# Kernel tuning notes

Hardware: AMD Instinct MI355X
Metric: run time of the kernel (lower is better)

The kernel has to match this reference:

```python
import jax, jax.numpy as jnp
import numpy as np

W, H = 512, 512
SHIFT_NORM = 100.0
P = 1
WEIGHT = 10.0
EPS = 1e-16


def _cv_matrix(angle, scale, shift, cx, cy):
    # cv2.getRotationMatrix2D-style matrix (pixel coords) with extra x-shift.
    alpha = scale * jnp.cos(angle)
    beta = scale * jnp.sin(angle)
    row0 = jnp.stack([alpha, beta, (1.0 - alpha) * cx - beta * cy + shift], axis=-1)
    row1 = jnp.stack([-beta, alpha, beta * cx + (1.0 - alpha) * cy], axis=-1)
    return jnp.stack([row0, row1], axis=-2)  # [B,2,3]


def _normalize_transform(M, width, height):
    # Convert pixel-space affine to normalized [-1,1] coords (align_corners=True).
    a, b, tx = M[:, 0, 0], M[:, 0, 1], M[:, 0, 2]
    c, d, ty = M[:, 1, 0], M[:, 1, 1], M[:, 1, 2]
    sw = float(width - 1)
    sh = float(height - 1)
    A = a
    Bc = b * sh / sw
    Cc = a + b * sh / sw + 2.0 * tx / sw - 1.0
    D = c * sw / sh
    E = d
    Fc = c * sw / sh + d + 2.0 * ty / sh - 1.0
    row0 = jnp.stack([A, Bc, Cc], axis=-1)
    row1 = jnp.stack([D, E, Fc], axis=-1)
    return jnp.stack([row0, row1], axis=-2)  # [B,2,3]


def _affine_grid(T, height, width):
    # torch affine_grid, align_corners=True
    u = jnp.linspace(-1.0, 1.0, width, dtype=T.dtype)
    v = jnp.linspace(-1.0, 1.0, height, dtype=T.dtype)
    vv, uu = jnp.meshgrid(v, u, indexing='ij')
    base = jnp.stack([uu, vv, jnp.ones_like(uu)], axis=-1)  # [H,W,3]
    return jnp.einsum('bij,hwj->bhwi', T, base)  # [B,H,W,2] (x,y)


def _grid_sample(img, grid):
    # bilinear, zeros padding, align_corners=True. img [B,C,H,W], grid [B,Ho,Wo,2]
    B, C, Hi, Wi = img.shape
    x = (grid[..., 0] + 1.0) * (Wi - 1) / 2.0
    y = (grid[..., 1] + 1.0) * (Hi - 1) / 2.0
    x0 = jnp.floor(x)
    y0 = jnp.floor(y)
    wx1 = x - x0
    wy1 = y - y0
    wx0 = 1.0 - wx1
    wy0 = 1.0 - wy1

    def gather(xi, yi):
        valid = ((xi >= 0) & (xi < Wi) & (yi >= 0) & (yi < Hi)).astype(img.dtype)
        xc = jnp.clip(xi, 0, Wi - 1).astype(jnp.int32)
        yc = jnp.clip(yi, 0, Hi - 1).astype(jnp.int32)
        g = jax.vmap(lambda im, xb, yb, vb: im[:, yb, xb] * vb[None])
        return g(img, xc, yc, valid)  # [B,C,Ho,Wo]

    out = (gather(x0, y0) * (wx0 * wy0)[:, None]
           + gather(x0 + 1, y0) * (wx1 * wy0)[:, None]
           + gather(x0, y0 + 1) * (wx0 * wy1)[:, None]
           + gather(x0 + 1, y0 + 1) * (wx1 * wy1)[:, None])
    return out


def setup_inputs() -> dict:
    key = jax.random.key(0)
    k1, k2, k3 = jax.random.split(key, 3)
    theta = jax.random.normal(k1, (32, 3), dtype=jnp.float32)
    img_R = jax.random.normal(k2, (32, 3, H, W), dtype=jnp.float32)
    img_R_orig = jax.random.normal(k3, (32, 3, H, W), dtype=jnp.float32)
    return {"theta": theta, "img_R": img_R, "img_R_orig": img_R_orig}


def reference(theta, img_R, img_R_orig):
    cx, cy = W // 2, H // 2
    M = _cv_matrix(theta[:, 0], theta[:, 1], SHIFT_NORM * theta[:, 2], cx, cy)
    T = _normalize_transform(M, W, H)
    grid = _affine_grid(T, H, W)
    warped = _grid_sample(img_R_orig, grid)
    mask = jnp.ones((img_R.shape[0], 1, H, W), dtype=img_R.dtype)
    warped_mask = _grid_sample(mask, grid)[:, 0]  # [B,H,W]
    # p=1 norm over channel dim
    nrm = jnp.sum(jnp.abs(img_R - warped), axis=1)  # [B,H,W]
    num = jnp.sum(warped_mask * nrm, axis=(1, 2)) + EPS
    den = jnp.sum(warped_mask, axis=(1, 2)) + EPS
    losses = WEIGHT * num / den
    return jnp.mean(losses)
```

## Files before the change

kernel.cpp:

```cpp
#include <hip/hip_runtime.h>
#include <math.h>

#define IMG_W 512
#define IMG_H 512
#define NB 32
#define NC 3
#define PLANE (IMG_H * IMG_W)

#define TILE_W 32
#define TILE_H 32
#define TILES_X (IMG_W / TILE_W)
#define TILES_Y (IMG_H / TILE_H)
#define TILES_PER_B (TILES_X * TILES_Y)
#define NBLOCKS (NB * TILES_PER_B)

#define LDSC 4096
#define LDSF (3 * LDSC)

typedef float vfloat4 __attribute__((ext_vector_type(4)));


__global__ __launch_bounds__(256, 3) void recon_main(
    const float* __restrict__ theta,
    const float* __restrict__ img_R,
    const float* __restrict__ img_orig,
    float* __restrict__ ws)
{
    __shared__ __align__(16) float tileLds[LDSF + 8];
    __shared__ float snum[4];
    __shared__ float sden[4];

    const int lin  = blockIdx.x;
    const int k    = lin & 7;
    const int i    = lin >> 3;
    const int step = i >> 5;
    const int t    = i & 31;
    const int b    = (4 * k + step) & 31;
    const int chk  = ((b >> 2) - k) & 7;
    const int tile = chk * 32 + t;
    const int tx = (tile & (TILES_X - 1)) * TILE_W;
    const int ty = (tile >> 4) * TILE_H;
    const int gcan = b * TILES_PER_B + tile;

    const int tid  = threadIdx.x;
    const int trow = tid >> 3;
    const int tcol = (tid & 7) * 4;

    const int h  = ty + trow;
    const int w0 = tx + tcol;
    const int p0 = h * IMG_W + w0;

    const float* orig_b = img_orig + (size_t)b * NC * PLANE;
    const float* R_b    = img_R    + (size_t)b * NC * PLANE;

    const vfloat4 rv0 = *(const vfloat4*)(R_b + 0 * PLANE + p0);
    const vfloat4 rv1 = *(const vfloat4*)(R_b + 1 * PLANE + p0);
    const vfloat4 rv2 = *(const vfloat4*)(R_b + 2 * PLANE + p0);

    const float ang   = theta[b * 3 + 0];
    const float s     = theta[b * 3 + 1];
    const float shift = 100.0f * theta[b * 3 + 2];
    float sn, cs;
    sincosf(ang, &sn, &cs);
    const float alpha = s * cs;
    const float beta  = s * sn;
    const float tx_a = (1.0f - alpha) * 256.0f - beta * 256.0f + shift;
    const float ty_a = beta * 256.0f + (1.0f - alpha) * 256.0f;
    const float Cc = alpha + beta + 2.0f * tx_a / 511.0f - 1.0f;
    const float Fc = -beta + alpha + 2.0f * ty_a / 511.0f - 1.0f;
    const float X0 = 255.5f * (Cc + 1.0f - alpha - beta);
    const float Y0 = 255.5f * (Fc + 1.0f + beta - alpha);

    const float xb = X0 + alpha * (float)w0 + beta * (float)h;
    const float yb = Y0 - beta * (float)w0 + alpha * (float)h;

    int   xi0a[4], xi1a[4], yi0a[4], yi1a[4];
    float w00[4], w10[4], w01[4], w11[4], mk[4];
    float den_acc = 0.0f;

#pragma unroll
    for (int j = 0; j < 4; ++j) {
        const float x = xb + alpha * (float)j;
        const float y = yb - beta  * (float)j;
        const float x0f = floorf(x), y0f = floorf(y);
        const float fx1 = x - x0f,  fy1 = y - y0f;
        const float fx0 = 1.0f - fx1, fy0 = 1.0f - fy1;
        const float vx0 = (x0f >=  0.0f && x0f <= 511.0f) ? 1.0f : 0.0f;
        const float vx1 = (x0f >= -1.0f && x0f <= 510.0f) ? 1.0f : 0.0f;
        const float vy0 = (y0f >=  0.0f && y0f <= 511.0f) ? 1.0f : 0.0f;
        const float vy1 = (y0f >= -1.0f && y0f <= 510.0f) ? 1.0f : 0.0f;
        xi0a[j] = (int)fminf(fmaxf(x0f,        0.0f), 511.0f);
        xi1a[j] = (int)fminf(fmaxf(x0f + 1.0f, 0.0f), 511.0f);
        yi0a[j] = (int)fminf(fmaxf(y0f,        0.0f), 511.0f);
        yi1a[j] = (int)fminf(fmaxf(y0f + 1.0f, 0.0f), 511.0f);
        w00[j] = fx0 * fy0 * vx0 * vy0;
        w10[j] = fx1 * fy0 * vx1 * vy0;
        w01[j] = fx0 * fy1 * vx0 * vy1;
        w11[j] = fx1 * fy1 * vx1 * vy1;
        mk[j]  = w00[j] + w10[j] + w01[j] + w11[j];
        den_acc += mk[j];
    }

    const float fx_lo = (float)tx, fx_hi = (float)(tx + TILE_W - 1);
    const float fy_lo = (float)ty, fy_hi = (float)(ty + TILE_H - 1);
    const float cxA = X0 + alpha * fx_lo + beta * fy_lo;
    const float cxB = X0 + alpha * fx_hi + beta * fy_lo;
    const float cxC = X0 + alpha * fx_lo + beta * fy_hi;
    const float cxD = X0 + alpha * fx_hi + beta * fy_hi;
    const float cyA = Y0 - beta * fx_lo + alpha * fy_lo;
    const float cyB = Y0 - beta * fx_hi + alpha * fy_lo;
    const float cyC = Y0 - beta * fx_lo + alpha * fy_hi;
    const float cyD = Y0 - beta * fx_hi + alpha * fy_hi;
    const float min_x = fminf(fminf(cxA, cxB), fminf(cxC, cxD));
    const float max_x = fmaxf(fmaxf(cxA, cxB), fmaxf(cxC, cxD));
    const float min_y = fminf(fminf(cyA, cyB), fminf(cyC, cyD));
    const float max_y = fmaxf(fmaxf(cyA, cyB), fmaxf(cyC, cyD));

    int xlo = (int)floorf(min_x);
    int xhi = (int)floorf(max_x) + 1;
    xlo = min(max(xlo, 0), 511);
    xhi = min(max(xhi, 0), 511);
    xlo &= ~3;
    int ylo = (int)floorf(min_y);
    int yhi = (int)floorf(max_y) + 1;
    ylo = min(max(ylo, 0), 511);
    yhi = min(max(yhi, 0), 511);

    const int bw = xhi - xlo + 1;
    const int bh = yhi - ylo + 1;
    int stride = (bw + 3) & ~3;
    if (((stride >> 2) & 1) == 0) stride += 4;
    const int nq4 = stride >> 2;
    const bool staged = (stride * bh <= LDSC) && (nq4 <= 32);

    float nrm[4] = {0.0f, 0.0f, 0.0f, 0.0f};

    if (staged) {
        int l00[4], l01[4], u0x[4];
#pragma unroll
        for (int j = 0; j < 4; ++j) {
            const int r0 = (yi0a[j] - ylo) * stride - xlo;
            const int r1 = (yi1a[j] - ylo) * stride - xlo;
            l00[j] = r0 + xi0a[j];
            l01[j] = r1 + xi0a[j];
            u0x[j] = xi1a[j] - xi0a[j];
        }
        int qq, r00, rstep;
        if (nq4 <= 8)       { qq = tid & 7;  r00 = tid >> 3; rstep = 32; }
        else if (nq4 <= 16) { qq = tid & 15; r00 = tid >> 4; rstep = 16; }
        else                { qq = tid & 31; r00 = tid >> 5; rstep = 8;  }
        const int col = xlo + (qq << 2);
        if (col <= xhi) {
            for (int r = r00; r < bh; r += rstep) {
                const float* src = orig_b + (ylo + r) * IMG_W + col;
                float* dst = &tileLds[r * stride + (qq << 2)];
#pragma unroll
                for (int c = 0; c < NC; ++c)
                    *(vfloat4*)(dst + c * LDSC) = *(const vfloat4*)(src + c * PLANE);
            }
        }
        __syncthreads();

#pragma unroll
        for (int c = 0; c < NC; ++c) {
            const vfloat4 rv = (c == 0) ? rv0 : (c == 1) ? rv1 : rv2;
            const float rj[4] = {rv.x, rv.y, rv.z, rv.w};
            const float* buf = &tileLds[c * LDSC];
#pragma unroll
            for (int j = 0; j < 4; ++j) {
                const float a0 = buf[l00[j]];
                const float a1 = buf[l00[j] + 1];
                const float b0 = buf[l01[j]];
                const float b1 = buf[l01[j] + 1];
                const float s10 = u0x[j] ? a1 : a0;
                const float s11 = u0x[j] ? b1 : b0;
                const float warped = a0 * w00[j] + s10 * w10[j]
                                   + b0 * w01[j] + s11 * w11[j];
                nrm[j] += fabsf(rj[j] - warped);
            }
        }
    } else {
        int a0i[4], a1i[4], sl0[4], sl1[4];
#pragma unroll
        for (int j = 0; j < 4; ++j) {
            const int xc = min(xi0a[j], 510);
            a0i[j] = yi0a[j] * IMG_W + xc;
            a1i[j] = yi1a[j] * IMG_W + xc;
            sl0[j] = xi0a[j] - xc;
            sl1[j] = xi1a[j] - xc;
        }
#pragma unroll
        for (int c = 0; c < NC; ++c) {
            const float* plane = orig_b + c * PLANE;
            const vfloat4 rv = (c == 0) ? rv0 : (c == 1) ? rv1 : rv2;
            const float rj[4] = {rv.x, rv.y, rv.z, rv.w};
#pragma unroll
            for (int j = 0; j < 4; ++j) {
                const float2 t0 = *(const float2*)(plane + a0i[j]);
                const float2 t1 = *(const float2*)(plane + a1i[j]);
                const float s00 = sl0[j] ? t0.y : t0.x;
                const float s10 = sl1[j] ? t0.y : t0.x;
                const float s01 = sl0[j] ? t1.y : t1.x;
                const float s11 = sl1[j] ? t1.y : t1.x;
                const float warped = s00 * w00[j] + s10 * w10[j]
                                   + s01 * w01[j] + s11 * w11[j];
                nrm[j] += fabsf(rj[j] - warped);
            }
        }
    }

    float num_acc = 0.0f;
#pragma unroll
    for (int j = 0; j < 4; ++j) num_acc += mk[j] * nrm[j];

#pragma unroll
    for (int off = 32; off > 0; off >>= 1) {
        num_acc += __shfl_down(num_acc, off);
        den_acc += __shfl_down(den_acc, off);
    }

    const int wave = threadIdx.x >> 6;
    const int lane = threadIdx.x & 63;
    if (lane == 0) { snum[wave] = num_acc; sden[wave] = den_acc; }
    __syncthreads();
    if (threadIdx.x == 0) {
        ws[gcan]           = snum[0] + snum[1] + snum[2] + snum[3];
        ws[NBLOCKS + gcan] = sden[0] + sden[1] + sden[2] + sden[3];
    }
}

__global__ __launch_bounds__(256) void recon_final(
    const float* __restrict__ ws,
    float* __restrict__ out)
{
    __shared__ float sloss[NB];
    const int t = threadIdx.x;
    const int b = t >> 3;
    const int j = t & 7;

    float n = 0.0f, d = 0.0f;
    for (int k = 0; k < 32; ++k) {
        const int tile = j * 32 + k;
        const int g    = b * TILES_PER_B + tile;
        n += ws[g];
        d += ws[NBLOCKS + g];
    }
#pragma unroll
    for (int off = 4; off > 0; off >>= 1) {
        n += __shfl_down(n, off);
        d += __shfl_down(d, off);
    }
    if (j == 0) sloss[b] = 10.0f * (n + 1e-16f) / (d + 1e-16f);
    __syncthreads();
    if (t == 0) {
        float L = 0.0f;
#pragma unroll
        for (int i = 0; i < NB; ++i) L += sloss[i];
        out[0] = L * (1.0f / (float)NB);
    }
}

extern "C" void kernel_launch(void* const* d_in, const int* in_sizes, int n_in,
                              void* d_out, int out_size, void* d_ws, size_t ws_size,
                              hipStream_t stream) {
    const float* theta    = (const float*)d_in[0];
    const float* img_R    = (const float*)d_in[1];
    const float* img_orig = (const float*)d_in[2];
    float* out = (float*)d_out;
    float* ws  = (float*)d_ws;

    recon_main<<<NBLOCKS, 256, 0, stream>>>(theta, img_R, img_orig, ws);
    recon_final<<<1, 256, 0, stream>>>(ws, out);
}
```

Baseline: 219.2 us.

## Double-buffer per-channel LDS staging to overlap global loads with compute

The staged path now loads one channel at a time into two ping-pong LDS buffers instead of all three channels at once. Global loads for the next channel are issued into registers before computing the current channel, so memory latency overlaps with the bilinear math. The smaller LDS footprint allows raising launch bounds from 3 to 4 blocks per CU for higher occupancy. In exchange it adds extra __syncthreads and register pressure from 8 prefetch vectors, and it caps staged rows at 8*rstep, which may send some tiles to the unstaged path.

```diff
diff --git a/kernel.cpp b/kernel.cpp
--- a/kernel.cpp
+++ b/kernel.cpp
@@ -15,18 +15,17 @@
 #define NBLOCKS (NB * TILES_PER_B)
 
 #define LDSC 4096
-#define LDSF (3 * LDSC)
 
 typedef float vfloat4 __attribute__((ext_vector_type(4)));
 
 
-__global__ __launch_bounds__(256, 3) void recon_main(
+__global__ __launch_bounds__(256, 4) void recon_main(
     const float* __restrict__ theta,
     const float* __restrict__ img_R,
     const float* __restrict__ img_orig,
     float* __restrict__ ws)
 {
-    __shared__ __align__(16) float tileLds[LDSF + 8];
+    __shared__ __align__(16) float tileLds[2 * LDSC + 8];
     __shared__ float snum[4];
     __shared__ float sden[4];
 
@@ -131,7 +130,12 @@
     int stride = (bw + 3) & ~3;
     if (((stride >> 2) & 1) == 0) stride += 4;
     const int nq4 = stride >> 2;
-    const bool staged = (stride * bh <= LDSC) && (nq4 <= 32);
+
+    int qq, r00, rstep;
+    if (nq4 <= 8)       { qq = tid & 7;  r00 = tid >> 3; rstep = 32; }
+    else if (nq4 <= 16) { qq = tid & 15; r00 = tid >> 4; rstep = 16; }
+    else                { qq = tid & 31; r00 = tid >> 5; rstep = 8;  }
+    const bool staged = (stride * bh <= LDSC) && (nq4 <= 32) && (bh <= (rstep << 3));
 
     float nrm[4] = {0.0f, 0.0f, 0.0f, 0.0f};
 
@@ -145,40 +149,65 @@
             l01[j] = r1 + xi0a[j];
             u0x[j] = xi1a[j] - xi0a[j];
         }
-        int qq, r00, rstep;
-        if (nq4 <= 8)       { qq = tid & 7;  r00 = tid >> 3; rstep = 32; }
-        else if (nq4 <= 16) { qq = tid & 15; r00 = tid >> 4; rstep = 16; }
-        else                { qq = tid & 31; r00 = tid >> 5; rstep = 8;  }
         const int col = xlo + (qq << 2);
-        if (col <= xhi) {
-            for (int r = r00; r < bh; r += rstep) {
-                const float* src = orig_b + (ylo + r) * IMG_W + col;
-                float* dst = &tileLds[r * stride + (qq << 2)];
-#pragma unroll
-                for (int c = 0; c < NC; ++c)
-                    *(vfloat4*)(dst + c * LDSC) = *(const vfloat4*)(src + c * PLANE);
-            }
-        }
+        const bool doload = (col <= xhi);
+        float* bufA = tileLds;
+        float* bufB = tileLds + LDSC;
+
+        vfloat4 pf[8];
+
+#define ISSUE_LOADS(C)                                                        \
+        _Pragma("unroll")                                                     \
+        for (int u = 0; u < 8; ++u) {                                         \
+            const int r = r00 + u * rstep;                                    \
+            if (doload && r < bh)                                             \
+                pf[u] = *(const vfloat4*)(orig_b + (C) * PLANE                \
+                                          + (ylo + r) * IMG_W + col);         \
+        }
+#define WRITE_LDS(BUF)                                                        \
+        _Pragma("unroll")                                                     \
+        for (int u = 0; u < 8; ++u) {                                         \
+            const int r = r00 + u * rstep;                                    \
+            if (doload && r < bh)                                             \
+                *(vfloat4*)(&(BUF)[r * stride + (qq << 2)]) = pf[u];          \
+        }
+#define COMPUTE_CH(BUF, RV)                                                   \
+        {                                                                     \
+            const vfloat4 rv = (RV);                                          \
+            const float rj[4] = {rv.x, rv.y, rv.z, rv.w};                     \
+            _Pragma("unroll")                                                 \
+            for (int j = 0; j < 4; ++j) {                                     \
+                const float a0 = (BUF)[l00[j]];                               \
+                const float a1 = (BUF)[l00[j] + 1];                           \
+                const float b0 = (BUF)[l01[j]];                               \
+                const float b1 = (BUF)[l01[j] + 1];                           \
+                const float s10 = u0x[j] ? a1 : a0;                           \
+                const float s11 = u0x[j] ? b1 : b0;                           \
+                const float warped = a0 * w00[j] + s10 * w10[j]               \
+                                   + b0 * w01[j] + s11 * w11[j];              \
+                nrm[j] += fabsf(rj[j] - warped);                              \
+            }                                                                 \
+        }
+
+        ISSUE_LOADS(0)
+        WRITE_LDS(bufA)
         __syncthreads();
 
-#pragma unroll
-        for (int c = 0; c < NC; ++c) {
-            const vfloat4 rv = (c == 0) ? rv0 : (c == 1) ? rv1 : rv2;
-            const float rj[4] = {rv.x, rv.y, rv.z, rv.w};
-            const float* buf = &tileLds[c * LDSC];
-#pragma unroll
-            for (int j = 0; j < 4; ++j) {
-                const float a0 = buf[l00[j]];
-                const float a1 = buf[l00[j] + 1];
-                const float b0 = buf[l01[j]];
-                const float b1 = buf[l01[j] + 1];
-                const float s10 = u0x[j] ? a1 : a0;
-                const float s11 = u0x[j] ? b1 : b0;
-                const float warped = a0 * w00[j] + s10 * w10[j]
-                                   + b0 * w01[j] + s11 * w11[j];
-                nrm[j] += fabsf(rj[j] - warped);
-            }
-        }
+        ISSUE_LOADS(1)
+        COMPUTE_CH(bufA, rv0)
+        WRITE_LDS(bufB)
+        __syncthreads();
+
+        ISSUE_LOADS(2)
+        COMPUTE_CH(bufB, rv1)
+        WRITE_LDS(bufA)
+        __syncthreads();
+
+        COMPUTE_CH(bufA, rv2)
+
+#undef ISSUE_LOADS
+#undef WRITE_LDS
+#undef COMPUTE_CH
     } else {
         int a0i[4], a1i[4], sl0[4], sl1[4];
 #pragma unroll
```

After: 222.8 us. No clear change (+1.6%).

## Precompute per-batch affine constants, skip out-of-bounds tiles, prefetch staged rows early

Applied to the files above, without the earlier changes.

A new tiny kernel computes each batch's affine constants (alpha, beta, X0, Y0) once and stores them in the workspace, so the main kernel no longer runs sincos per block. Tiles whose warped footprint lies entirely outside the source image now skip all loads and math, including the img_R reads. For staged tiles, the first four rows of source data are loaded into registers before the per-pixel weight computation, so global latency overlaps with arithmetic. This adds an extra kernel launch, more register pressure from the prefetch buffers, and a dependency on workspace ordering.

```diff
diff --git a/kernel.cpp b/kernel.cpp
--- a/kernel.cpp
+++ b/kernel.cpp
@@ -16,12 +16,37 @@
 
 #define LDSC 4096
 #define LDSF (3 * LDSC)
+#define CONS_OFF (2 * NBLOCKS)
 
 typedef float vfloat4 __attribute__((ext_vector_type(4)));
 
 
+__global__ __launch_bounds__(64) void recon_prep(
+    const float* __restrict__ theta, float* __restrict__ ws)
+{
+    const int b = threadIdx.x;
+    if (b < NB) {
+        const float ang   = theta[b * 3 + 0];
+        const float s     = theta[b * 3 + 1];
+        const float shift = 100.0f * theta[b * 3 + 2];
+        float sn, cs;
+        sincosf(ang, &sn, &cs);
+        const float alpha = s * cs;
+        const float beta  = s * sn;
+        const float tx_a = (1.0f - alpha) * 256.0f - beta * 256.0f + shift;
+        const float ty_a = beta * 256.0f + (1.0f - alpha) * 256.0f;
+        const float Cc = alpha + beta + 2.0f * tx_a / 511.0f - 1.0f;
+        const float Fc = -beta + alpha + 2.0f * ty_a / 511.0f - 1.0f;
+        const float X0 = 255.5f * (Cc + 1.0f - alpha - beta);
+        const float Y0 = 255.5f * (Fc + 1.0f + beta - alpha);
+        ws[CONS_OFF + 4 * b + 0] = alpha;
+        ws[CONS_OFF + 4 * b + 1] = beta;
+        ws[CONS_OFF + 4 * b + 2] = X0;
+        ws[CONS_OFF + 4 * b + 3] = Y0;
+    }
+}
+
 __global__ __launch_bounds__(256, 3) void recon_main(
-    const float* __restrict__ theta,
     const float* __restrict__ img_R,
     const float* __restrict__ img_orig,
     float* __restrict__ ws)
@@ -53,53 +78,8 @@
     const float* orig_b = img_orig + (size_t)b * NC * PLANE;
     const float* R_b    = img_R    + (size_t)b * NC * PLANE;
 
-    const vfloat4 rv0 = *(const vfloat4*)(R_b + 0 * PLANE + p0);
-    const vfloat4 rv1 = *(const vfloat4*)(R_b + 1 * PLANE + p0);
-    const vfloat4 rv2 = *(const vfloat4*)(R_b + 2 * PLANE + p0);
-
-    const float ang   = theta[b * 3 + 0];
-    const float s     = theta[b * 3 + 1];
-    const float shift = 100.0f * theta[b * 3 + 2];
-    float sn, cs;
-    sincosf(ang, &sn, &cs);
-    const float alpha = s * cs;
-    const float beta  = s * sn;
-    const float tx_a = (1.0f - alpha) * 256.0f - beta * 256.0f + shift;
-    const float ty_a = beta * 256.0f + (1.0f - alpha) * 256.0f;
-    const float Cc = alpha + beta + 2.0f * tx_a / 511.0f - 1.0f;
-    const float Fc = -beta + alpha + 2.0f * ty_a / 511.0f - 1.0f;
-    const float X0 = 255.5f * (Cc + 1.0f - alpha - beta);
-    const float Y0 = 255.5f * (Fc + 1.0f + beta - alpha);
-
-    const float xb = X0 + alpha * (float)w0 + beta * (float)h;
-    const float yb = Y0 - beta * (float)w0 + alpha * (float)h;
-
-    int   xi0a[4], xi1a[4], yi0a[4], yi1a[4];
-    float w00[4], w10[4], w01[4], w11[4], mk[4];
-    float den_acc = 0.0f;
-
-#pragma unroll
-    for (int j = 0; j < 4; ++j) {
-        const float x = xb + alpha * (float)j;
-        const float y = yb - beta  * (float)j;
-        const float x0f = floorf(x), y0f = floorf(y);
-        const float fx1 = x - x0f,  fy1 = y - y0f;
-        const float fx0 = 1.0f - fx1, fy0 = 1.0f - fy1;
-        const float vx0 = (x0f >=  0.0f && x0f <= 511.0f) ? 1.0f : 0.0f;
-        const float vx1 = (x0f >= -1.0f && x0f <= 510.0f) ? 1.0f : 0.0f;
-        const float vy0 = (y0f >=  0.0f && y0f <= 511.0f) ? 1.0f : 0.0f;
-        const float vy1 = (y0f >= -1.0f && y0f <= 510.0f) ? 1.0f : 0.0f;
-        xi0a[j] = (int)fminf(fmaxf(x0f,        0.0f), 511.0f);
-        xi1a[j] = (int)fminf(fmaxf(x0f + 1.0f, 0.0f), 511.0f);
-        yi0a[j] = (int)fminf(fmaxf(y0f,        0.0f), 511.0f);
-        yi1a[j] = (int)fminf(fmaxf(y0f + 1.0f, 0.0f), 511.0f);
-        w00[j] = fx0 * fy0 * vx0 * vy0;
-        w10[j] = fx1 * fy0 * vx1 * vy0;
-        w01[j] = fx0 * fy1 * vx0 * vy1;
-        w11[j] = fx1 * fy1 * vx1 * vy1;
-        mk[j]  = w00[j] + w10[j] + w01[j] + w11[j];
-        den_acc += mk[j];
-    }
+    const vfloat4 cb = *(const vfloat4*)(ws + CONS_OFF + 4 * b);
+    const float alpha = cb.x, beta = cb.y, X0 = cb.z, Y0 = cb.w;
 
     const float fx_lo = (float)tx, fx_hi = (float)(tx + TILE_W - 1);
     const float fy_lo = (float)ty, fy_hi = (float)(ty + TILE_H - 1);
@@ -116,102 +96,213 @@
     const float min_y = fminf(fminf(cyA, cyB), fminf(cyC, cyD));
     const float max_y = fmaxf(fmaxf(cyA, cyB), fmaxf(cyC, cyD));
 
-    int xlo = (int)floorf(min_x);
-    int xhi = (int)floorf(max_x) + 1;
-    xlo = min(max(xlo, 0), 511);
-    xhi = min(max(xhi, 0), 511);
-    xlo &= ~3;
-    int ylo = (int)floorf(min_y);
-    int yhi = (int)floorf(max_y) + 1;
-    ylo = min(max(ylo, 0), 511);
-    yhi = min(max(yhi, 0), 511);
-
-    const int bw = xhi - xlo + 1;
-    const int bh = yhi - ylo + 1;
-    int stride = (bw + 3) & ~3;
-    if (((stride >> 2) & 1) == 0) stride += 4;
-    const int nq4 = stride >> 2;
-    const bool staged = (stride * bh <= LDSC) && (nq4 <= 32);
-
-    float nrm[4] = {0.0f, 0.0f, 0.0f, 0.0f};
-
-    if (staged) {
-        int l00[4], l01[4], u0x[4];
-#pragma unroll
-        for (int j = 0; j < 4; ++j) {
-            const int r0 = (yi0a[j] - ylo) * stride - xlo;
-            const int r1 = (yi1a[j] - ylo) * stride - xlo;
-            l00[j] = r0 + xi0a[j];
-            l01[j] = r1 + xi0a[j];
-            u0x[j] = xi1a[j] - xi0a[j];
-        }
+    const bool oob = (max_x < 0.0f) || (min_x > 511.0f) ||
+                     (max_y < 0.0f) || (min_y > 511.0f);
+
+    float num_acc = 0.0f, den_acc = 0.0f;
+
+    if (!oob) {
+        int xlo = (int)floorf(min_x);
+        int xhi = (int)floorf(max_x) + 1;
+        xlo = min(max(xlo, 0), 511);
+        xhi = min(max(xhi, 0), 511);
+        xlo &= ~3;
+        int ylo = (int)floorf(min_y);
+        int yhi = (int)floorf(max_y) + 1;
+        ylo = min(max(ylo, 0), 511);
+        yhi = min(max(yhi, 0), 511);
+
+        const int bw = xhi - xlo + 1;
+        const int bh = yhi - ylo + 1;
+        int stride = (bw + 3) & ~3;
+        if (((stride >> 2) & 1) == 0) stride += 4;
+        const int nq4 = stride >> 2;
+        const bool staged = (stride * bh <= LDSC) && (nq4 <= 32);
+
         int qq, r00, rstep;
         if (nq4 <= 8)       { qq = tid & 7;  r00 = tid >> 3; rstep = 32; }
         else if (nq4 <= 16) { qq = tid & 15; r00 = tid >> 4; rstep = 16; }
         else                { qq = tid & 31; r00 = tid >> 5; rstep = 8;  }
         const int col = xlo + (qq << 2);
-        if (col <= xhi) {
-            for (int r = r00; r < bh; r += rstep) {
-                const float* src = orig_b + (ylo + r) * IMG_W + col;
-                float* dst = &tileLds[r * stride + (qq << 2)];
-#pragma unroll
-                for (int c = 0; c < NC; ++c)
-                    *(vfloat4*)(dst + c * LDSC) = *(const vfloat4*)(src + c * PLANE);
+        const bool doload = staged && (col <= xhi);
+
+        const float xb = X0 + alpha * (float)w0 + beta * (float)h;
+        const float yb = Y0 - beta * (float)w0 + alpha * (float)h;
+
+        int   xi0a[4], xi1a[4], yi0a[4], yi1a[4];
+        float w00[4], w10[4], w01[4], w11[4], mk[4];
+        float nrm[4] = {0.0f, 0.0f, 0.0f, 0.0f};
+
+        if (staged) {
+            const int r1 = r00 + rstep, r2 = r00 + 2 * rstep, r3 = r00 + 3 * rstep;
+            const bool v0 = doload && (r00 < bh);
+            const bool v1 = doload && (r1  < bh);
+            const bool v2 = doload && (r2  < bh);
+            const bool v3 = doload && (r3  < bh);
+            vfloat4 pf0[3], pf1[3], pf2[3], pf3[3];
+            const float* src0 = orig_b + (ylo + r00) * IMG_W + col;
+            const float* src1 = orig_b + (ylo + r1)  * IMG_W + col;
+            const float* src2 = orig_b + (ylo + r2)  * IMG_W + col;
+            const float* src3 = orig_b + (ylo + r3)  * IMG_W + col;
+            if (v0) {
+#pragma unroll
+                for (int c = 0; c < NC; ++c) pf0[c] = *(const vfloat4*)(src0 + c * PLANE);
+            }
+            if (v1) {
+#pragma unroll
+                for (int c = 0; c < NC; ++c) pf1[c] = *(const vfloat4*)(src1 + c * PLANE);
+            }
+            if (v2) {
+#pragma unroll
+                for (int c = 0; c < NC; ++c) pf2[c] = *(const vfloat4*)(src2 + c * PLANE);
+            }
+            if (v3) {
+#pragma unroll
+                for (int c = 0; c < NC; ++c) pf3[c] = *(const vfloat4*)(src3 + c * PLANE);
+            }
+            const vfloat4 rv0 = *(const vfloat4*)(R_b + 0 * PLANE + p0);
+            const vfloat4 rv1 = *(const vfloat4*)(R_b + 1 * PLANE + p0);
+            const vfloat4 rv2 = *(const vfloat4*)(R_b + 2 * PLANE + p0);
+
+#pragma unroll
+            for (int j = 0; j < 4; ++j) {
+                const float x = xb + alpha * (float)j;
+                const float y = yb - beta  * (float)j;
+                const float x0f = floorf(x), y0f = floorf(y);
+                const float fx1 = x - x0f,  fy1 = y - y0f;
+                const float fx0 = 1.0f - fx1, fy0 = 1.0f - fy1;
+                const float vx0 = (x0f >=  0.0f && x0f <= 511.0f) ? 1.0f : 0.0f;
+                const float vx1 = (x0f >= -1.0f && x0f <= 510.0f) ? 1.0f : 0.0f;
+                const float vy0 = (y0f >=  0.0f && y0f <= 511.0f) ? 1.0f : 0.0f;
+                const float vy1 = (y0f >= -1.0f && y0f <= 510.0f) ? 1.0f : 0.0f;
+                xi0a[j] = (int)fminf(fmaxf(x0f,        0.0f), 511.0f);
+                xi1a[j] = (int)fminf(fmaxf(x0f + 1.0f, 0.0f), 511.0f);
+                yi0a[j] = (int)fminf(fmaxf(y0f,        0.0f), 511.0f);
+                yi1a[j] = (int)fminf(fmaxf(y0f + 1.0f, 0.0f), 511.0f);
+                w00[j] = fx0 * fy0 * vx0 * vy0;
+                w10[j] = fx1 * fy0 * vx1 * vy0;
+                w01[j] = fx0 * fy1 * vx0 * vy1;
+                w11[j] = fx1 * fy1 * vx1 * vy1;
+                mk[j]  = w00[j] + w10[j] + w01[j] + w11[j];
+                den_acc += mk[j];
+            }
+            int l00[4], l01[4], u0x[4];
+#pragma unroll
+            for (int j = 0; j < 4; ++j) {
+                const int r0i = (yi0a[j] - ylo) * stride - xlo;
+                const int r1i = (yi1a[j] - ylo) * stride - xlo;
+                l00[j] = r0i + xi0a[j];
+                l01[j] = r1i + xi0a[j];
+                u0x[j] = xi1a[j] - xi0a[j];
+            }
+
+            if (v0) {
+                float* dst = &tileLds[r00 * stride + (qq << 2)];
+#pragma unroll
+                for (int c = 0; c < NC; ++c) *(vfloat4*)(dst + c * LDSC) = pf0[c];
+            }
+            if (v1) {
+                float* dst = &tileLds[r1 * stride + (qq << 2)];
+#pragma unroll
+                for (int c = 0; c < NC; ++c) *(vfloat4*)(dst + c * LDSC) = pf1[c];
+            }
+            if (v2) {
+                float* dst = &tileLds[r2 * stride + (qq << 2)];
+#pragma unroll
+                for (int c = 0; c < NC; ++c) *(vfloat4*)(dst + c * LDSC) = pf2[c];
+            }
+            if (v3) {
+                float* dst = &tileLds[r3 * stride + (qq << 2)];
+#pragma unroll
+                for (int c = 0; c < NC; ++c) *(vfloat4*)(dst + c * LDSC) = pf3[c];
+            }
+            if (doload) {
+                for (int r = r00 + 4 * rstep; r < bh; r += rstep) {
+                    const float* src = orig_b + (ylo + r) * IMG_W + col;
+                    float* dst = &tileLds[r * stride + (qq << 2)];
+#pragma unroll
+                    for (int c = 0; c < NC; ++c)
+                        *(vfloat4*)(dst + c * LDSC) = *(const vfloat4*)(src + c * PLANE);
+                }
+            }
+            __syncthreads();
+
+#pragma unroll
+            for (int c = 0; c < NC; ++c) {
+                const vfloat4 rv = (c == 0) ? rv0 : (c == 1) ? rv1 : rv2;
+                const float rj[4] = {rv.x, rv.y, rv.z, rv.w};
+                const float* buf = &tileLds[c * LDSC];
+#pragma unroll
+                for (int j = 0; j < 4; ++j) {
+                    const float a0 = buf[l00[j]];
+                    const float a1 = buf[l00[j] + 1];
+                    const float b0 = buf[l01[j]];
+                    const float b1 = buf[l01[j] + 1];
+                    const float s10 = u0x[j] ? a1 : a0;
+                    const float s11 = u0x[j] ? b1 : b0;
+                    const float warped = a0 * w00[j] + s10 * w10[j]
+                                       + b0 * w01[j] + s11 * w11[j];
+                    nrm[j] += fabsf(rj[j] - warped);
+                }
+            }
+        } else {
+            const vfloat4 rv0 = *(const vfloat4*)(R_b + 0 * PLANE + p0);
+            const vfloat4 rv1 = *(const vfloat4*)(R_b + 1 * PLANE + p0);
+            const vfloat4 rv2 = *(const vfloat4*)(R_b + 2 * PLANE + p0);
+#pragma unroll
+            for (int j = 0; j < 4; ++j) {
+                const float x = xb + alpha * (float)j;
+                const float y = yb - beta  * (float)j;
+                const float x0f = floorf(x), y0f = floorf(y);
+                const float fx1 = x - x0f,  fy1 = y - y0f;
+                const float fx0 = 1.0f - fx1, fy0 = 1.0f - fy1;
+                const float vx0 = (x0f >=  0.0f && x0f <= 511.0f) ? 1.0f : 0.0f;
+                const float vx1 = (x0f >= -1.0f && x0f <= 510.0f) ? 1.0f : 0.0f;
+                const float vy0 = (y0f >=  0.0f && y0f <= 511.0f) ? 1.0f : 0.0f;
+                const float vy1 = (y0f >= -1.0f && y0f <= 510.0f) ? 1.0f : 0.0f;
+                xi0a[j] = (int)fminf(fmaxf(x0f,        0.0f), 511.0f);
+                xi1a[j] = (int)fminf(fmaxf(x0f + 1.0f, 0.0f), 511.0f);
+                yi0a[j] = (int)fminf(fmaxf(y0f,        0.0f), 511.0f);
+                yi1a[j] = (int)fminf(fmaxf(y0f + 1.0f, 0.0f), 511.0f);
+                w00[j] = fx0 * fy0 * vx0 * vy0;
+                w10[j] = fx1 * fy0 * vx1 * vy0;
+                w01[j] = fx0 * fy1 * vx0 * vy1;
+                w11[j] = fx1 * fy1 * vx1 * vy1;
+                mk[j]  = w00[j] + w10[j] + w01[j] + w11[j];
+                den_acc += mk[j];
+            }
+            int a0i[4], a1i[4], sl0[4], sl1[4];
+#pragma unroll
+            for (int j = 0; j < 4; ++j) {
+                const int xc = min(xi0a[j], 510);
+                a0i[j] = yi0a[j] * IMG_W + xc;
+                a1i[j] = yi1a[j] * IMG_W + xc;
+                sl0[j] = xi0a[j] - xc;
+                sl1[j] = xi1a[j] - xc;
+            }
+#pragma unroll
+            for (int c = 0; c < NC; ++c) {
+                const float* plane = orig_b + c * PLANE;
+                const vfloat4 rv = (c == 0) ? rv0 : (c == 1) ? rv1 : rv2;
+                const float rj[4] = {rv.x, rv.y, rv.z, rv.w};
+#pragma unroll
+                for (int j = 0; j < 4; ++j) {
+                    const float2 t0 = *(const float2*)(plane + a0i[j]);
+                    const float2 t1 = *(const float2*)(plane + a1i[j]);
+                    const float s00 = sl0[j] ? t0.y : t0.x;
+                    const float s10 = sl1[j] ? t0.y : t0.x;
+                    const float s01 = sl0[j] ? t1.y : t1.x;
+                    const float s11 = sl1[j] ? t1.y : t1.x;
+                    const float warped = s00 * w00[j] + s10 * w10[j]
+                                       + s01 * w01[j] + s11 * w11[j];
+                    nrm[j] += fabsf(rj[j] - warped);
+                }
             }
         }
-        __syncthreads();
-
-#pragma unroll
-        for (int c = 0; c < NC; ++c) {
-            const vfloat4 rv = (c == 0) ? rv0 : (c == 1) ? rv1 : rv2;
-            const float rj[4] = {rv.x, rv.y, rv.z, rv.w};
-            const float* buf = &tileLds[c * LDSC];
-#pragma unroll
-            for (int j = 0; j < 4; ++j) {
-                const float a0 = buf[l00[j]];
-                const float a1 = buf[l00[j] + 1];
-                const float b0 = buf[l01[j]];
-                const float b1 = buf[l01[j] + 1];
-                const float s10 = u0x[j] ? a1 : a0;
-                const float s11 = u0x[j] ? b1 : b0;
-                const float warped = a0 * w00[j] + s10 * w10[j]
-                                   + b0 * w01[j] + s11 * w11[j];
-                nrm[j] += fabsf(rj[j] - warped);
-            }
-        }
-    } else {
-        int a0i[4], a1i[4], sl0[4], sl1[4];
-#pragma unroll
-        for (int j = 0; j < 4; ++j) {
-            const int xc = min(xi0a[j], 510);
-            a0i[j] = yi0a[j] * IMG_W + xc;
-            a1i[j] = yi1a[j] * IMG_W + xc;
-            sl0[j] = xi0a[j] - xc;
-            sl1[j] = xi1a[j] - xc;
-        }
-#pragma unroll
-        for (int c = 0; c < NC; ++c) {
-            const float* plane = orig_b + c * PLANE;
-            const vfloat4 rv = (c == 0) ? rv0 : (c == 1) ? rv1 : rv2;
-            const float rj[4] = {rv.x, rv.y, rv.z, rv.w};
-#pragma unroll
-            for (int j = 0; j < 4; ++j) {
-                const float2 t0 = *(const float2*)(plane + a0i[j]);
-                const float2 t1 = *(const float2*)(plane + a1i[j]);
-                const float s00 = sl0[j] ? t0.y : t0.x;
-                const float s10 = sl1[j] ? t0.y : t0.x;
-                const float s01 = sl0[j] ? t1.y : t1.x;
-                const float s11 = sl1[j] ? t1.y : t1.x;
-                const float warped = s00 * w00[j] + s10 * w10[j]
-                                   + s01 * w01[j] + s11 * w11[j];
-                nrm[j] += fabsf(rj[j] - warped);
-            }
-        }
-    }
-
-    float num_acc = 0.0f;
-#pragma unroll
-    for (int j = 0; j < 4; ++j) num_acc += mk[j] * nrm[j];
+
+#pragma unroll
+        for (int j = 0; j < 4; ++j) num_acc += mk[j] * nrm[j];
+    }
 
 #pragma unroll
     for (int off = 32; off > 0; off >>= 1) {
@@ -269,6 +360,7 @@
     float* out = (float*)d_out;
     float* ws  = (float*)d_ws;
 
-    recon_main<<<NBLOCKS, 256, 0, stream>>>(theta, img_R, img_orig, ws);
+    recon_prep<<<1, 64, 0, stream>>>(theta, ws);
+    recon_main<<<NBLOCKS, 256, 0, stream>>>(img_R, img_orig, ws);
     recon_final<<<1, 256, 0, stream>>>(ws, out);
 }
```

Result: no change. 216.6 us (-1.2%).
